# Kernel tuning notes

Measured on AMD Instinct MI355X. Metric: run time of the kernel, lower is better.

Reference implementation:

```python
import jax, jax.numpy as jnp
import numpy as np

N = 50000   # nodes
E = 800000  # edges (avg degree 16)
FIN = 128   # input node features
H = 4       # heads (conv1, conv2)
C = 64      # hidden_channels (per-head out dim)
SLOPE = 0.2
LN_EPS = 1e-5


def gatv2(x, src, dst, Wl, bl, Wr, br, att, bo, heads, outc, n):
    # GATv2Conv: e = att . LeakyReLU(x_l[src] + x_r[dst]); segment-softmax over dst; scatter-add alpha * x_l[src]
    xl = (x @ Wl + bl).reshape(n, heads, outc)
    xr = (x @ Wr + br).reshape(n, heads, outc)
    e = jax.nn.leaky_relu(xl[src] + xr[dst], SLOPE)          # [E, H, C]
    score = jnp.einsum('ehc,hc->eh', e, att)                 # [E, H]
    smax = jax.ops.segment_max(score, dst, num_segments=n)   # [N, H]
    ex = jnp.exp(score - smax[dst])
    denom = jax.ops.segment_sum(ex, dst, num_segments=n)
    alpha = ex / (denom[dst] + 1e-16)                        # [E, H]
    out = jax.ops.segment_sum(alpha[:, :, None] * xl[src], dst, num_segments=n)  # [N, H, C]
    return out.reshape(n, heads * outc) + bo                 # concat=True (default)


def layernorm(x, g, b):
    mu = x.mean(-1, keepdims=True)
    var = ((x - mu) ** 2).mean(-1, keepdims=True)
    return (x - mu) * jax.lax.rsqrt(var + LN_EPS) * g + b


def setup_inputs() -> dict:
    key = jax.random.key(0)
    ks = jax.random.split(key, 32)
    f32 = jnp.float32
    def nrm(k, shape, s):
        return jax.random.normal(k, shape, dtype=f32) * s
    inp = {}
    inp['x'] = jax.random.normal(ks[0], (N, FIN), dtype=f32)
    inp['edge_index'] = jax.random.randint(ks[1], (2, E), 0, N, dtype=jnp.int32)
    inp['batch'] = jnp.zeros((N,), dtype=jnp.int32)
    # conv1: 128 -> 4*64
    inp['W1l'] = nrm(ks[2], (FIN, H * C), 1.0 / np.sqrt(FIN))
    inp['b1l'] = jnp.zeros((H * C,), f32)
    inp['W1r'] = nrm(ks[3], (FIN, H * C), 1.0 / np.sqrt(FIN))
    inp['b1r'] = jnp.zeros((H * C,), f32)
    inp['a1'] = nrm(ks[4], (H, C), 1.0 / np.sqrt(C))
    inp['bo1'] = jnp.zeros((H * C,), f32)
    inp['ln1_g'] = jnp.ones((H * C,), f32)
    inp['ln1_b'] = jnp.zeros((H * C,), f32)
    # conv2: 256 -> 4*64
    inp['W2l'] = nrm(ks[5], (H * C, H * C), 1.0 / np.sqrt(H * C))
    inp['b2l'] = jnp.zeros((H * C,), f32)
    inp['W2r'] = nrm(ks[6], (H * C, H * C), 1.0 / np.sqrt(H * C))
    inp['b2r'] = jnp.zeros((H * C,), f32)
    inp['a2'] = nrm(ks[7], (H, C), 1.0 / np.sqrt(C))
    inp['bo2'] = jnp.zeros((H * C,), f32)
    inp['ln2_g'] = jnp.ones((H * C,), f32)
    inp['ln2_b'] = jnp.zeros((H * C,), f32)
    # conv3: 256 -> 1*64 (heads=1)
    inp['W3l'] = nrm(ks[8], (H * C, C), 1.0 / np.sqrt(H * C))
    inp['b3l'] = jnp.zeros((C,), f32)
    inp['W3r'] = nrm(ks[9], (H * C, C), 1.0 / np.sqrt(H * C))
    inp['b3r'] = jnp.zeros((C,), f32)
    inp['a3'] = nrm(ks[10], (1, C), 1.0 / np.sqrt(C))
    inp['bo3'] = jnp.zeros((C,), f32)
    inp['ln3_g'] = jnp.ones((C,), f32)
    inp['ln3_b'] = jnp.zeros((C,), f32)
    # final linear 64 -> 64
    inp['linW'] = nrm(ks[11], (C, C), 1.0 / np.sqrt(C))
    inp['linb'] = jnp.zeros((C,), f32)
    return inp


def reference(x, edge_index, batch,
              W1l, b1l, W1r, b1r, a1, bo1, ln1_g, ln1_b,
              W2l, b2l, W2r, b2r, a2, bo2, ln2_g, ln2_b,
              W3l, b3l, W3r, b3r, a3, bo3, ln3_g, ln3_b,
              linW, linb):
    src, dst = edge_index[0], edge_index[1]
    n = x.shape[0]
    h = gatv2(x, src, dst, W1l, b1l, W1r, b1r, a1, bo1, H, C, n)
    h = layernorm(h, ln1_g, ln1_b)
    h = gatv2(h, src, dst, W2l, b2l, W2r, b2r, a2, bo2, H, C, n)
    h = layernorm(h, ln2_g, ln2_b)
    h = gatv2(h, src, dst, W3l, b3l, W3r, b3r, a3, bo3, 1, C, n)
    h = layernorm(h, ln3_g, ln3_b)
    return h @ linW + linb
```

## Files before the change

kernel.cpp:

```cpp
#include <hip/hip_runtime.h>
#include <math.h>

#define LRELU_SLOPE 0.2f
#define L2E 1.4426950408889634f

typedef __attribute__((ext_vector_type(8))) short bf16x8;
typedef __attribute__((ext_vector_type(4))) float f32x4;
typedef __attribute__((ext_vector_type(2))) float f2;

__device__ __forceinline__ float fast_exp2(float x) {
  float r; asm("v_exp_f32 %0, %1" : "=v"(r) : "v"(x)); return r;
}

template<int CTRL>
__device__ __forceinline__ float dpp_add(float v) {
  int p = __builtin_amdgcn_update_dpp(0, __float_as_int(v), CTRL, 0xF, 0xF, true);
  return v + __int_as_float(p);
}
__device__ __forceinline__ float row16_sum(float v) {
  v = dpp_add<0xB1>(v);
  v = dpp_add<0x4E>(v);
  v = dpp_add<0x124>(v);
  v = dpp_add<0x128>(v);
  return v;
}

__device__ __forceinline__ unsigned short f2bf(float f) {
  unsigned u = __float_as_uint(f);
  return (unsigned short)((u + 0x7FFFu + ((u >> 16) & 1u)) >> 16);
}
__device__ __forceinline__ f2 bfpair(unsigned p) {
  f2 r;
  r.x = __uint_as_float(p << 16);
  r.y = __uint_as_float(p & 0xffff0000u);
  return r;
}

__global__ void wt_cvt_all(
    const float* __restrict__ W1l, const float* __restrict__ W1r,
    const float* __restrict__ W2l, const float* __restrict__ W2r,
    const float* __restrict__ W3l, const float* __restrict__ W3r,
    unsigned short* __restrict__ Wt1l, unsigned short* __restrict__ Wt1r,
    unsigned short* __restrict__ Wt2l, unsigned short* __restrict__ Wt2r,
    unsigned short* __restrict__ Wt3l, unsigned short* __restrict__ Wt3r) {
  const float* W; unsigned short* Wt; int K, N;
  switch (blockIdx.y) {
    case 0: W = W1l; Wt = Wt1l; K = 128; N = 256; break;
    case 1: W = W1r; Wt = Wt1r; K = 128; N = 256; break;
    case 2: W = W2l; Wt = Wt2l; K = 256; N = 256; break;
    case 3: W = W2r; Wt = Wt2r; K = 256; N = 256; break;
    case 4: W = W3l; Wt = Wt3l; K = 256; N = 64;  break;
    default: W = W3r; Wt = Wt3r; K = 256; N = 64; break;
  }
  int i = blockIdx.x * blockDim.x + threadIdx.x;
  int k8s = K / 8;
  int n = i / k8s, k8 = i - n * k8s;
  if (n >= N) return;
  unsigned short tmp[8];
#pragma unroll
  for (int j = 0; j < 8; ++j) tmp[j] = f2bf(W[(size_t)(k8 * 8 + j) * N + n]);
  *(bf16x8*)(Wt + (size_t)n * K + k8 * 8) = *(bf16x8*)tmp;
}

template<int K, bool CVT>
__global__ __launch_bounds__(256) void gemm_side(
    const void* __restrict__ Xsrc,
    const unsigned short* __restrict__ Wt0, const unsigned short* __restrict__ Wt1,
    const float* __restrict__ bias0, const float* __restrict__ bias1,
    unsigned short* __restrict__ Y0, unsigned short* __restrict__ Y1, int M) {
  constexpr int LDK = K + 8;
  constexpr int SMEM = (64 * LDK > 64 * 256) ? 64 * LDK : 64 * 256;
  __shared__ unsigned short smem[SMEM];
  unsigned short* As = smem;
  const int t = threadIdx.x, w = t >> 6, l = t & 63;
  const int lr = l & 15, lk = l >> 4;
  const int rowBase = blockIdx.x * 64;
  const int side = blockIdx.y;
  const unsigned short* Wt = side ? Wt1 : Wt0;
  const float* bias = side ? bias1 : bias0;
  unsigned short* Y = side ? Y1 : Y0;

  if constexpr (CVT) {
    const float* Xf = (const float*)Xsrc;
    constexpr int SPR = K / 4;
    constexpr int ITER = (64 * SPR) / 256;
#pragma unroll
    for (int i = 0; i < ITER; ++i) {
      int idx = i * 256 + t;
      int row = idx / SPR, seg = idx - row * SPR;
      int gr = rowBase + row; if (gr >= M) gr = M - 1;
      float4 v = *(const float4*)(Xf + (size_t)gr * K + seg * 4);
      ushort4 o;
      o.x = f2bf(v.x); o.y = f2bf(v.y); o.z = f2bf(v.z); o.w = f2bf(v.w);
      *(ushort4*)(As + row * LDK + seg * 4) = o;
    }
  } else {
    const unsigned short* Xb = (const unsigned short*)Xsrc;
    constexpr int SPR = K / 8;
    constexpr int ITER = (64 * SPR) / 256;
#pragma unroll
    for (int i = 0; i < ITER; ++i) {
      int idx = i * 256 + t;
      int row = idx / SPR, seg = idx - row * SPR;
      int gr = rowBase + row; if (gr >= M) gr = M - 1;
      *(uint4*)(As + row * LDK + seg * 8) = *(const uint4*)(Xb + (size_t)gr * K + seg * 8);
    }
  }
  __syncthreads();

  const int n0 = w * 64;

  f32x4 acc[4][4];
#pragma unroll
  for (int rt = 0; rt < 4; ++rt)
#pragma unroll
    for (int nt = 0; nt < 4; ++nt) acc[rt][nt] = (f32x4){0.f, 0.f, 0.f, 0.f};

  const unsigned short* bp = Wt + (size_t)(n0 + lr) * K + lk * 8;
  const unsigned short* ap = As + lr * LDK + lk * 8;

#pragma unroll
  for (int k0 = 0; k0 < K; k0 += 32) {
    bf16x8 a[4], b[4];
#pragma unroll
    for (int rt = 0; rt < 4; ++rt) a[rt] = *(const bf16x8*)(ap + rt * 16 * LDK + k0);
#pragma unroll
    for (int nt = 0; nt < 4; ++nt) b[nt] = *(const bf16x8*)(bp + nt * 16 * K + k0);
#pragma unroll
    for (int rt = 0; rt < 4; ++rt)
#pragma unroll
      for (int nt = 0; nt < 4; ++nt)
        acc[rt][nt] = __builtin_amdgcn_mfma_f32_16x16x32_bf16(a[rt], b[nt], acc[rt][nt], 0, 0, 0);
  }

  unsigned short* ybuf = smem;
  __syncthreads();
#pragma unroll
  for (int nt = 0; nt < 4; ++nt) {
    float bv = bias[n0 + nt * 16 + lr];
#pragma unroll
    for (int rt = 0; rt < 4; ++rt)
#pragma unroll
      for (int r = 0; r < 4; ++r)
        ybuf[(rt * 16 + lk * 4 + r) * 256 + n0 + nt * 16 + lr] =
            f2bf(acc[rt][nt][r] + bv);
  }
  __syncthreads();
#pragma unroll
  for (int i = 0; i < 8; ++i) {
    int boff = (i * 256 + t) * 16;
    int row = boff >> 9;
    int col = boff & 511;
    int rg = rowBase + row;
    if (rg < M)
      *(uint4*)((char*)Y + (((size_t)rg << 9) + col)) =
          *(const uint4*)((const char*)ybuf + boff);
  }
}

template<int K>
__global__ __launch_bounds__(256) void gemm_n64(
    const unsigned short* __restrict__ Xb,
    const unsigned short* __restrict__ Wt0, const unsigned short* __restrict__ Wt1,
    const float* __restrict__ bias0, const float* __restrict__ bias1,
    unsigned short* __restrict__ Y0, unsigned short* __restrict__ Y1, int M) {
  __shared__ unsigned short ybuf[64 * 64];
  const int side = blockIdx.y;
  const unsigned short* Wt = side ? Wt1 : Wt0;
  const float* bias = side ? bias1 : bias0;
  unsigned short* Y = side ? Y1 : Y0;
  const int t = threadIdx.x, w = t >> 6, l = t & 63;
  const int lr = l & 15, lk = l >> 4;
  const int rowBase = blockIdx.x * 64 + w * 16;

  f32x4 acc[4];
#pragma unroll
  for (int nt = 0; nt < 4; ++nt) acc[nt] = (f32x4){0.f, 0.f, 0.f, 0.f};

  int arow = rowBase + lr; if (arow >= M) arow = M - 1;
  const unsigned short* ap = Xb + (size_t)arow * K + lk * 8;
  const unsigned short* bp = Wt + (size_t)lr * K + lk * 8;

#pragma unroll
  for (int k0 = 0; k0 < K; k0 += 32) {
    bf16x8 a = *(const bf16x8*)(ap + k0);
    bf16x8 b[4];
#pragma unroll
    for (int nt = 0; nt < 4; ++nt) b[nt] = *(const bf16x8*)(bp + nt * 16 * K + k0);
#pragma unroll
    for (int nt = 0; nt < 4; ++nt)
      acc[nt] = __builtin_amdgcn_mfma_f32_16x16x32_bf16(a, b[nt], acc[nt], 0, 0, 0);
  }

#pragma unroll
  for (int nt = 0; nt < 4; ++nt) {
    float bv = bias[nt * 16 + lr];
#pragma unroll
    for (int r = 0; r < 4; ++r)
      ybuf[(w * 16 + lk * 4 + r) * 64 + nt * 16 + lr] = f2bf(acc[nt][r] + bv);
  }
  __syncthreads();

  const size_t base = (size_t)blockIdx.x * 64 * 64;
#pragma unroll
  for (int i = 0; i < 2; ++i) {
    int idx = i * 256 + t;
    int off = idx * 8;
    int row = off >> 6;
    if (blockIdx.x * 64 + row < M)
      *(uint4*)(Y + base + off) = *(const uint4*)(ybuf + off);
  }
}

__global__ void hist_deg(const int* __restrict__ dst, int* __restrict__ deg, int Ee) {
  int e = blockIdx.x * blockDim.x + threadIdx.x;
  if (e < Ee) atomicAdd(&deg[dst[e]], 1);
}

__global__ void scan_blk(const int* __restrict__ deg, int* __restrict__ rowptr,
                         int* __restrict__ bsum, int n) {
  __shared__ int sm[256];
  const int b = blockIdx.x, t = threadIdx.x;
  const int i = b * 256 + t;
  const int v = (i < n) ? deg[i] : 0;
  sm[t] = v;
  __syncthreads();
#pragma unroll
  for (int off = 1; off < 256; off <<= 1) {
    int x = (t >= off) ? sm[t - off] : 0;
    __syncthreads();
    sm[t] += x;
    __syncthreads();
  }
  if (i < n) rowptr[i] = sm[t] - v;
  if (t == 255) bsum[b] = sm[255];
}

__global__ void scan_top(const int* __restrict__ bsum, int* __restrict__ boff,
                         int* __restrict__ rowptr, int nb, int n) {
  __shared__ int sm[1024];
  const int t = threadIdx.x;
  const int v = (t < nb) ? bsum[t] : 0;
  sm[t] = v;
  __syncthreads();
#pragma unroll
  for (int off = 1; off < 1024; off <<= 1) {
    int x = (t >= off) ? sm[t - off] : 0;
    __syncthreads();
    sm[t] += x;
    __syncthreads();
  }
  if (t < nb) boff[t] = sm[t] - v;
  if (t == 1023) rowptr[n] = sm[1023];
}

__global__ void scan_add(int* __restrict__ rowptr, const int* __restrict__ boff, int n) {
  int i = blockIdx.x * 256 + threadIdx.x;
  if (i < n) rowptr[i] += boff[blockIdx.x];
}

__global__ void fill_csr(const int* __restrict__ src, const int* __restrict__ dst,
                         const int* __restrict__ rowptr, int* __restrict__ deg,
                         int* __restrict__ csr_src, int Ee) {
  int e = blockIdx.x * blockDim.x + threadIdx.x;
  if (e < Ee) {
    int d = dst[e];
    int p = atomicSub(&deg[d], 1) - 1;
    csr_src[rowptr[d] + p] = src[e];
  } else if (e < Ee + 16) {
    csr_src[e] = 0;
  }
}

__global__ __launch_bounds__(256) void gat_fused4(
    const unsigned short* __restrict__ xlb, const unsigned short* __restrict__ xrb,
    const float* __restrict__ att,
    const int* __restrict__ rowptr, const int* __restrict__ csr_src,
    const float* __restrict__ bo, const float* __restrict__ gam,
    const float* __restrict__ bet, unsigned short* __restrict__ outp, int n) {
  const int t = threadIdx.x;
  const int wv = t >> 6, lane = t & 63;
  const int node = blockIdx.x * 4 + wv;
  if (node >= n) return;
  const int cb = lane * 4;
  const unsigned loff = (unsigned)lane << 3;
  const char* xl8 = (const char*)xlb;

  uint2 xp = *(const uint2*)((const char*)xrb + (((unsigned)node << 9) + loff));
  const f2 xr0 = bfpair(xp.x), xr1 = bfpair(xp.y);
  const float4 a4 = *(const float4*)(att + cb);
  const f2 at0 = {a4.x * L2E, a4.y * L2E};
  const f2 at1 = {a4.z * L2E, a4.w * L2E};

  const int r0 = rowptr[node], r1 = rowptr[node + 1];
  float s = 0.f;
  f2 o0 = {0.f, 0.f}, o1 = {0.f, 0.f};

  if (r0 < r1) {
#define GOFF(idx) ((((unsigned)csr_src[idx]) << 9) + loff)
    uint2 p0 = *(const uint2*)(xl8 + GOFF(r0));
    uint2 p1 = *(const uint2*)(xl8 + GOFF(r0 + 1));
    uint2 p2 = *(const uint2*)(xl8 + GOFF(r0 + 2));
    uint2 p3 = *(const uint2*)(xl8 + GOFF(r0 + 3));
    for (int i = r0; i < r1; i += 4) {
      const uint2 c0 = p0, c1 = p1, c2 = p2, c3 = p3;
      if (i + 4 < r1) {
        p0 = *(const uint2*)(xl8 + GOFF(i + 4));
        p1 = *(const uint2*)(xl8 + GOFF(i + 5));
        p2 = *(const uint2*)(xl8 + GOFF(i + 6));
        p3 = *(const uint2*)(xl8 + GOFF(i + 7));
      }
      const f2 v00 = bfpair(c0.x), v01 = bfpair(c0.y);
      const f2 v10 = bfpair(c1.x), v11 = bfpair(c1.y);
      const f2 v20 = bfpair(c2.x), v21 = bfpair(c2.y);
      const f2 v30 = bfpair(c3.x), v31 = bfpair(c3.y);

      f2 e;
      f2 q0, q1, q2, q3;
      e = v00 + xr0; e = __builtin_elementwise_max(e, e * LRELU_SLOPE); q0 = e * at0;
      e = v01 + xr1; e = __builtin_elementwise_max(e, e * LRELU_SLOPE); q0 += e * at1;
      e = v10 + xr0; e = __builtin_elementwise_max(e, e * LRELU_SLOPE); q1 = e * at0;
      e = v11 + xr1; e = __builtin_elementwise_max(e, e * LRELU_SLOPE); q1 += e * at1;
      e = v20 + xr0; e = __builtin_elementwise_max(e, e * LRELU_SLOPE); q2 = e * at0;
      e = v21 + xr1; e = __builtin_elementwise_max(e, e * LRELU_SLOPE); q2 += e * at1;
      e = v30 + xr0; e = __builtin_elementwise_max(e, e * LRELU_SLOPE); q3 = e * at0;
      e = v31 + xr1; e = __builtin_elementwise_max(e, e * LRELU_SLOPE); q3 += e * at1;

      float s0 = row16_sum(q0.x + q0.y);
      float s1 = row16_sum(q1.x + q1.y);
      float s2 = row16_sum(q2.x + q2.y);
      float s3 = row16_sum(q3.x + q3.y);
      if (i + 1 >= r1) s1 = -INFINITY;
      if (i + 2 >= r1) s2 = -INFINITY;
      if (i + 3 >= r1) s3 = -INFINITY;
      const float w0 = fast_exp2(s0), w1 = fast_exp2(s1);
      const float w2 = fast_exp2(s2), w3 = fast_exp2(s3);
      s += (w0 + w1) + (w2 + w3);
      o0 += v00 * w0; o1 += v01 * w0;
      o0 += v10 * w1; o1 += v11 * w1;
      o0 += v20 * w2; o1 += v21 * w2;
      o0 += v30 * w3; o1 += v31 * w3;
    }
#undef GOFF
  }

  const float inv = 1.f / (s + 1e-16f);
  const float4 b4 = *(const float4*)(bo + cb);
  const float v0 = fmaf(o0.x, inv, b4.x);
  const float v1 = fmaf(o0.y, inv, b4.y);
  const float v2 = fmaf(o1.x, inv, b4.z);
  const float v3 = fmaf(o1.y, inv, b4.w);

  float ls = row16_sum(v0 + v1 + v2 + v3);
  ls += __shfl_xor(ls, 16);
  ls += __shfl_xor(ls, 32);
  const float mu = ls * (1.f / 256.f);
  const float d0 = v0 - mu, d1 = v1 - mu, d2 = v2 - mu, d3 = v3 - mu;
  float q = row16_sum(d0 * d0 + d1 * d1 + d2 * d2 + d3 * d3);
  q += __shfl_xor(q, 16);
  q += __shfl_xor(q, 32);
  const float rs = rsqrtf(q * (1.f / 256.f) + 1e-5f);

  const float4 g4 = *(const float4*)(gam + cb);
  const float4 e4 = *(const float4*)(bet + cb);
  ushort4 res;
  res.x = f2bf(fmaf(d0 * rs, g4.x, e4.x));
  res.y = f2bf(fmaf(d1 * rs, g4.y, e4.y));
  res.z = f2bf(fmaf(d2 * rs, g4.z, e4.z));
  res.w = f2bf(fmaf(d3 * rs, g4.w, e4.w));
  *(ushort4*)((char*)outp + (((unsigned)node << 9) + loff)) = res;
}

__global__ __launch_bounds__(512) void gat1_lin(
    const unsigned short* __restrict__ xlb, const unsigned short* __restrict__ xrb,
    const float* __restrict__ att,
    const int* __restrict__ rowptr, const int* __restrict__ csr_src,
    const float* __restrict__ bo, const float* __restrict__ gam,
    const float* __restrict__ bet,
    const float* __restrict__ linW, const float* __restrict__ linb,
    float* __restrict__ outp, int n) {
  const int t = threadIdx.x;
  const int wv = t >> 6, lane = t & 63;
  const int grp = lane >> 3, c8 = lane & 7;
  __shared__ float lw[64][64];
  __shared__ float hbuf[8][64];
  for (int i = t; i < 4096; i += 512) lw[i >> 6][i & 63] = linW[i];

  const int node = blockIdx.x * 8 + wv;
  const bool active = node < n;
  const int cb = c8 * 8;
  const unsigned loff = (unsigned)c8 << 4;
  const char* xl8 = (const char*)xlb;

  f2 xr2[4];
  int r0 = 0, r1 = 0;
  if (active) {
    uint4 p = *(const uint4*)((const char*)xrb + (((unsigned)node << 7) + loff));
    xr2[0] = bfpair(p.x); xr2[1] = bfpair(p.y); xr2[2] = bfpair(p.z); xr2[3] = bfpair(p.w);
    r0 = rowptr[node];
    r1 = rowptr[node + 1];
  } else {
#pragma unroll
    for (int j = 0; j < 4; ++j) xr2[j] = (f2){0.f, 0.f};
  }
  f2 at2[4];
  {
    float4 a0 = *(const float4*)(att + cb);
    float4 a1 = *(const float4*)(att + cb + 4);
    at2[0] = (f2){a0.x * L2E, a0.y * L2E}; at2[1] = (f2){a0.z * L2E, a0.w * L2E};
    at2[2] = (f2){a1.x * L2E, a1.y * L2E}; at2[3] = (f2){a1.z * L2E, a1.w * L2E};
  }

  float s = 0.f;
  f2 o2[4];
#pragma unroll
  for (int j = 0; j < 4; ++j) o2[j] = (f2){0.f, 0.f};

  uint4 vpk = {0u, 0u, 0u, 0u};
  {
    int i0 = r0 + grp;
    if (i0 < r1) vpk = *(const uint4*)(xl8 + ((((unsigned)csr_src[i0]) << 7) + loff));
  }
  bool valid = (r0 + grp) < r1;

  for (int base = r0; base < r1; base += 8) {
    const uint4 pc = vpk;
    const bool vld = valid;
    int inext = base + 8 + grp;
    valid = inext < r1;
    if (valid) vpk = *(const uint4*)(xl8 + ((((unsigned)csr_src[inext]) << 7) + loff));

    f2 v0 = bfpair(pc.x), v1 = bfpair(pc.y), v2 = bfpair(pc.z), v3 = bfpair(pc.w);
    f2 e0 = v0 + xr2[0]; e0 = __builtin_elementwise_max(e0, e0 * LRELU_SLOPE);
    f2 e1 = v1 + xr2[1]; e1 = __builtin_elementwise_max(e1, e1 * LRELU_SLOPE);
    f2 e2 = v2 + xr2[2]; e2 = __builtin_elementwise_max(e2, e2 * LRELU_SLOPE);
    f2 e3 = v3 + xr2[3]; e3 = __builtin_elementwise_max(e3, e3 * LRELU_SLOPE);
    f2 sc2 = e0 * at2[0];
    sc2 += e1 * at2[1];
    sc2 += e2 * at2[2];
    sc2 += e3 * at2[3];
    float sc = sc2.x + sc2.y;
    sc = dpp_add<0xB1>(sc);
    sc = dpp_add<0x4E>(sc);
    sc += __shfl_xor(sc, 4);
    if (!vld) sc = -INFINITY;
    const float w = fast_exp2(sc);
    s += w;
    o2[0] += v0 * w;
    o2[1] += v1 * w;
    o2[2] += v2 * w;
    o2[3] += v3 * w;
  }

  float o[8] = {o2[0].x, o2[0].y, o2[1].x, o2[1].y, o2[2].x, o2[2].y, o2[3].x, o2[3].y};
#pragma unroll
  for (int off = 8; off < 64; off <<= 1) {
#pragma unroll
    for (int i = 0; i < 8; ++i) o[i] += __shfl_xor(o[i], off);
    s += __shfl_xor(s, off);
  }

  const float inv = 1.f / (s + 1e-16f);
  float val[8];
  {
    float4 b0 = *(const float4*)(bo + cb);
    float4 b1 = *(const float4*)(bo + cb + 4);
    val[0] = fmaf(o[0], inv, b0.x); val[1] = fmaf(o[1], inv, b0.y);
    val[2] = fmaf(o[2], inv, b0.z); val[3] = fmaf(o[3], inv, b0.w);
    val[4] = fmaf(o[4], inv, b1.x); val[5] = fmaf(o[5], inv, b1.y);
    val[6] = fmaf(o[6], inv, b1.z); val[7] = fmaf(o[7], inv, b1.w);
  }

  float ls = 0.f;
#pragma unroll
  for (int i = 0; i < 8; ++i) ls += val[i];
  ls = dpp_add<0xB1>(ls);
  ls = dpp_add<0x4E>(ls);
  ls += __shfl_xor(ls, 4);
  float mu = ls * (1.f / 64.f);
  float d[8], q = 0.f;
#pragma unroll
  for (int i = 0; i < 8; ++i) { d[i] = val[i] - mu; q = fmaf(d[i], d[i], q); }
  q = dpp_add<0xB1>(q);
  q = dpp_add<0x4E>(q);
  q += __shfl_xor(q, 4);
  float var = q * (1.f / 64.f);
  const float rs = rsqrtf(var + 1e-5f);

  if (grp == 0) {
    float4 g0 = *(const float4*)(gam + cb);
    float4 g1 = *(const float4*)(gam + cb + 4);
    float4 e0 = *(const float4*)(bet + cb);
    float4 e1 = *(const float4*)(bet + cb + 4);
    float* hb = &hbuf[wv][cb];
    hb[0] = fmaf(d[0] * rs, g0.x, e0.x); hb[1] = fmaf(d[1] * rs, g0.y, e0.y);
    hb[2] = fmaf(d[2] * rs, g0.z, e0.z); hb[3] = fmaf(d[3] * rs, g0.w, e0.w);
    hb[4] = fmaf(d[4] * rs, g1.x, e1.x); hb[5] = fmaf(d[5] * rs, g1.y, e1.y);
    hb[6] = fmaf(d[6] * rs, g1.z, e1.z); hb[7] = fmaf(d[7] * rs, g1.w, e1.w);
  }
  __syncthreads();

  float acc = linb[lane];
#pragma unroll 8
  for (int k = 0; k < 64; ++k) acc = fmaf(hbuf[wv][k], lw[k][lane], acc);
  if (active) outp[(size_t)node * 64 + lane] = acc;
}

extern "C" void kernel_launch(void* const* d_in, const int* in_sizes, int n_in,
                              void* d_out, int out_size, void* d_ws, size_t ws_size,
                              hipStream_t stream) {
  const float* x    = (const float*)d_in[0];
  const int*   eidx = (const int*)d_in[1];
  const int Nn = in_sizes[0] / 128;
  const int Ee = in_sizes[1] / 2;
  const int* src = eidx;
  const int* dst = eidx + Ee;

  const float* W1l = (const float*)d_in[3];  const float* b1l = (const float*)d_in[4];
  const float* W1r = (const float*)d_in[5];  const float* b1r = (const float*)d_in[6];
  const float* a1  = (const float*)d_in[7];  const float* bo1 = (const float*)d_in[8];
  const float* g1  = (const float*)d_in[9];  const float* be1 = (const float*)d_in[10];
  const float* W2l = (const float*)d_in[11]; const float* b2l = (const float*)d_in[12];
  const float* W2r = (const float*)d_in[13]; const float* b2r = (const float*)d_in[14];
  const float* a2  = (const float*)d_in[15]; const float* bo2 = (const float*)d_in[16];
  const float* g2  = (const float*)d_in[17]; const float* be2 = (const float*)d_in[18];
  const float* W3l = (const float*)d_in[19]; const float* b3l = (const float*)d_in[20];
  const float* W3r = (const float*)d_in[21]; const float* b3r = (const float*)d_in[22];
  const float* a3  = (const float*)d_in[23]; const float* bo3 = (const float*)d_in[24];
  const float* g3  = (const float*)d_in[25]; const float* be3 = (const float*)d_in[26];
  const float* linW = (const float*)d_in[27]; const float* linb = (const float*)d_in[28];

  char* ws = (char*)d_ws;
  unsigned short* xl   = (unsigned short*)ws; ws += (size_t)Nn * 256 * 2;
  unsigned short* xr   = (unsigned short*)ws; ws += (size_t)Nn * 256 * 2;
  unsigned short* Xb   = (unsigned short*)ws; ws += (size_t)Nn * 256 * 2;
  unsigned short* Wt1l = (unsigned short*)ws; ws += 256 * 128 * 2;
  unsigned short* Wt1r = (unsigned short*)ws; ws += 256 * 128 * 2;
  unsigned short* Wt2l = (unsigned short*)ws; ws += 256 * 256 * 2;
  unsigned short* Wt2r = (unsigned short*)ws; ws += 256 * 256 * 2;
  unsigned short* Wt3l = (unsigned short*)ws; ws += 64 * 256 * 2;
  unsigned short* Wt3r = (unsigned short*)ws; ws += 64 * 256 * 2;
  int*   deg    = (int*)ws;    ws += (size_t)Nn * 4;
  int*   rowptr = (int*)ws;    ws += (size_t)(Nn + 1) * 4;
  int*   bsum   = (int*)ws;    ws += 1024 * 4;
  int*   boff   = (int*)ws;    ws += 1024 * 4;
  int*   csr_src= (int*)ws;    ws += (size_t)(Ee + 16) * 4;

  const int eblk = (Ee + 255) / 256;
  const int nblk = (Nn + 255) / 256;

  hipMemsetAsync(deg, 0, (size_t)Nn * 4, stream);
  hist_deg<<<eblk, 256, 0, stream>>>(dst, deg, Ee);
  wt_cvt_all<<<dim3(32, 6), 256, 0, stream>>>(W1l, W1r, W2l, W2r, W3l, W3r,
                                              Wt1l, Wt1r, Wt2l, Wt2r, Wt3l, Wt3r);
  scan_blk<<<nblk, 256, 0, stream>>>(deg, rowptr, bsum, Nn);
  scan_top<<<1, 1024, 0, stream>>>(bsum, boff, rowptr, nblk, Nn);
  scan_add<<<nblk, 256, 0, stream>>>(rowptr, boff, Nn);
  fill_csr<<<(Ee + 16 + 255) / 256, 256, 0, stream>>>(src, dst, rowptr, deg, csr_src, Ee);

  const int gdblk = (Nn + 63) / 64;

  gemm_side<128, true><<<dim3(gdblk, 2), 256, 0, stream>>>(x, Wt1l, Wt1r, b1l, b1r, xl, xr, Nn);
  gat_fused4<<<(Nn + 3) / 4, 256, 0, stream>>>(xl, xr, a1, rowptr, csr_src, bo1, g1, be1, Xb, Nn);

  gemm_side<256, false><<<dim3(gdblk, 2), 256, 0, stream>>>(Xb, Wt2l, Wt2r, b2l, b2r, xl, xr, Nn);
  gat_fused4<<<(Nn + 3) / 4, 256, 0, stream>>>(xl, xr, a2, rowptr, csr_src, bo2, g2, be2, Xb, Nn);

  gemm_n64<256><<<dim3(gdblk, 2), 256, 0, stream>>>(Xb, Wt3l, Wt3r, b3l, b3r, xl, xr, Nn);
  gat1_lin<<<(Nn + 7) / 8, 512, 0, stream>>>(xl, xr, a3, rowptr, csr_src, bo3, g3, be3,
                                             linW, linb, (float*)d_out, Nn);
}
```

Measured before the change: 375.2 us.

## Split wave into two half-waves processing alternate edges with 16-byte gathers

The 4-head GAT aggregation kernel now has each 32-lane half-wave handle alternate edges, with each lane loading 8 bf16 features (16 bytes) instead of 4. Per-head score reductions shrink to 8-lane groups, and the two halves' partial sums are combined by cross-half shuffles at the end. The intent is to use wider vector loads and more gathers in flight per wave, cutting loop iterations per node. The cost is extra shuffles, more registers, and wasted lanes on nodes with odd or small degree.

```diff
diff --git a/kernel.cpp b/kernel.cpp
--- a/kernel.cpp
+++ b/kernel.cpp
@@ -22,6 +22,12 @@
   v = dpp_add<0x4E>(v);
   v = dpp_add<0x124>(v);
   v = dpp_add<0x128>(v);
+  return v;
+}
+__device__ __forceinline__ float grp8_sum(float v) {
+  v = dpp_add<0xB1>(v);
+  v = dpp_add<0x4E>(v);
+  v += __shfl_xor(v, 4);
   return v;
 }
 
@@ -282,93 +288,108 @@
   const int wv = t >> 6, lane = t & 63;
   const int node = blockIdx.x * 4 + wv;
   if (node >= n) return;
-  const int cb = lane * 4;
-  const unsigned loff = (unsigned)lane << 3;
+  const int half = lane >> 5;
+  const int c32 = lane & 31;
+  const int cb = c32 * 8;
+  const unsigned loff = (unsigned)c32 << 4;
   const char* xl8 = (const char*)xlb;
 
-  uint2 xp = *(const uint2*)((const char*)xrb + (((unsigned)node << 9) + loff));
-  const f2 xr0 = bfpair(xp.x), xr1 = bfpair(xp.y);
-  const float4 a4 = *(const float4*)(att + cb);
-  const f2 at0 = {a4.x * L2E, a4.y * L2E};
-  const f2 at1 = {a4.z * L2E, a4.w * L2E};
+  uint4 xp = *(const uint4*)((const char*)xrb + (((unsigned)node << 9) + loff));
+  const f2 xr0 = bfpair(xp.x), xr1 = bfpair(xp.y), xr2 = bfpair(xp.z), xr3 = bfpair(xp.w);
+  const float4 a0 = *(const float4*)(att + cb);
+  const float4 a1 = *(const float4*)(att + cb + 4);
+  const f2 at0 = {a0.x * L2E, a0.y * L2E};
+  const f2 at1 = {a0.z * L2E, a0.w * L2E};
+  const f2 at2 = {a1.x * L2E, a1.y * L2E};
+  const f2 at3 = {a1.z * L2E, a1.w * L2E};
 
   const int r0 = rowptr[node], r1 = rowptr[node + 1];
   float s = 0.f;
-  f2 o0 = {0.f, 0.f}, o1 = {0.f, 0.f};
+  f2 o0 = {0.f, 0.f}, o1 = {0.f, 0.f}, o2 = {0.f, 0.f}, o3 = {0.f, 0.f};
 
   if (r0 < r1) {
 #define GOFF(idx) ((((unsigned)csr_src[idx]) << 9) + loff)
-    uint2 p0 = *(const uint2*)(xl8 + GOFF(r0));
-    uint2 p1 = *(const uint2*)(xl8 + GOFF(r0 + 1));
-    uint2 p2 = *(const uint2*)(xl8 + GOFF(r0 + 2));
-    uint2 p3 = *(const uint2*)(xl8 + GOFF(r0 + 3));
-    for (int i = r0; i < r1; i += 4) {
-      const uint2 c0 = p0, c1 = p1, c2 = p2, c3 = p3;
-      if (i + 4 < r1) {
-        p0 = *(const uint2*)(xl8 + GOFF(i + 4));
-        p1 = *(const uint2*)(xl8 + GOFF(i + 5));
-        p2 = *(const uint2*)(xl8 + GOFF(i + 6));
-        p3 = *(const uint2*)(xl8 + GOFF(i + 7));
+    uint4 p0 = *(const uint4*)(xl8 + GOFF(r0 + 0 + half));
+    uint4 p1 = *(const uint4*)(xl8 + GOFF(r0 + 2 + half));
+    uint4 p2 = *(const uint4*)(xl8 + GOFF(r0 + 4 + half));
+    uint4 p3 = *(const uint4*)(xl8 + GOFF(r0 + 6 + half));
+    for (int i = r0; i < r1; i += 8) {
+      const uint4 c0 = p0, c1 = p1, c2 = p2, c3 = p3;
+      if (i + 8 < r1) {
+        p0 = *(const uint4*)(xl8 + GOFF(i + 8 + half));
+        p1 = *(const uint4*)(xl8 + GOFF(i + 10 + half));
+        p2 = *(const uint4*)(xl8 + GOFF(i + 12 + half));
+        p3 = *(const uint4*)(xl8 + GOFF(i + 14 + half));
       }
-      const f2 v00 = bfpair(c0.x), v01 = bfpair(c0.y);
-      const f2 v10 = bfpair(c1.x), v11 = bfpair(c1.y);
-      const f2 v20 = bfpair(c2.x), v21 = bfpair(c2.y);
-      const f2 v30 = bfpair(c3.x), v31 = bfpair(c3.y);
-
-      f2 e;
-      f2 q0, q1, q2, q3;
-      e = v00 + xr0; e = __builtin_elementwise_max(e, e * LRELU_SLOPE); q0 = e * at0;
-      e = v01 + xr1; e = __builtin_elementwise_max(e, e * LRELU_SLOPE); q0 += e * at1;
-      e = v10 + xr0; e = __builtin_elementwise_max(e, e * LRELU_SLOPE); q1 = e * at0;
-      e = v11 + xr1; e = __builtin_elementwise_max(e, e * LRELU_SLOPE); q1 += e * at1;
-      e = v20 + xr0; e = __builtin_elementwise_max(e, e * LRELU_SLOPE); q2 = e * at0;
-      e = v21 + xr1; e = __builtin_elementwise_max(e, e * LRELU_SLOPE); q2 += e * at1;
-      e = v30 + xr0; e = __builtin_elementwise_max(e, e * LRELU_SLOPE); q3 = e * at0;
-      e = v31 + xr1; e = __builtin_elementwise_max(e, e * LRELU_SLOPE); q3 += e * at1;
-
-      float s0 = row16_sum(q0.x + q0.y);
-      float s1 = row16_sum(q1.x + q1.y);
-      float s2 = row16_sum(q2.x + q2.y);
-      float s3 = row16_sum(q3.x + q3.y);
-      if (i + 1 >= r1) s1 = -INFINITY;
-      if (i + 2 >= r1) s2 = -INFINITY;
-      if (i + 3 >= r1) s3 = -INFINITY;
-      const float w0 = fast_exp2(s0), w1 = fast_exp2(s1);
-      const float w2 = fast_exp2(s2), w3 = fast_exp2(s3);
-      s += (w0 + w1) + (w2 + w3);
-      o0 += v00 * w0; o1 += v01 * w0;
-      o0 += v10 * w1; o1 += v11 * w1;
-      o0 += v20 * w2; o1 += v21 * w2;
-      o0 += v30 * w3; o1 += v31 * w3;
+#pragma unroll
+      for (int k = 0; k < 4; ++k) {
+        const uint4 ck = (k == 0) ? c0 : (k == 1) ? c1 : (k == 2) ? c2 : c3;
+        const f2 v0 = bfpair(ck.x), v1 = bfpair(ck.y);
+        const f2 v2 = bfpair(ck.z), v3 = bfpair(ck.w);
+        f2 e, q;
+        e = v0 + xr0; e = __builtin_elementwise_max(e, e * LRELU_SLOPE); q = e * at0;
+        e = v1 + xr1; e = __builtin_elementwise_max(e, e * LRELU_SLOPE); q += e * at1;
+        e = v2 + xr2; e = __builtin_elementwise_max(e, e * LRELU_SLOPE); q += e * at2;
+        e = v3 + xr3; e = __builtin_elementwise_max(e, e * LRELU_SLOPE); q += e * at3;
+        float sc = grp8_sum(q.x + q.y);
+        const int ek = i + 2 * k + half;
+        if (ek >= r1) sc = -INFINITY;
+        const float w = fast_exp2(sc);
+        s += w;
+        o0 += v0 * w;
+        o1 += v1 * w;
+        o2 += v2 * w;
+        o3 += v3 * w;
+      }
     }
 #undef GOFF
+    o0.x += __shfl_xor(o0.x, 32); o0.y += __shfl_xor(o0.y, 32);
+    o1.x += __shfl_xor(o1.x, 32); o1.y += __shfl_xor(o1.y, 32);
+    o2.x += __shfl_xor(o2.x, 32); o2.y += __shfl_xor(o2.y, 32);
+    o3.x += __shfl_xor(o3.x, 32); o3.y += __shfl_xor(o3.y, 32);
+    s += __shfl_xor(s, 32);
   }
 
   const float inv = 1.f / (s + 1e-16f);
-  const float4 b4 = *(const float4*)(bo + cb);
-  const float v0 = fmaf(o0.x, inv, b4.x);
-  const float v1 = fmaf(o0.y, inv, b4.y);
-  const float v2 = fmaf(o1.x, inv, b4.z);
-  const float v3 = fmaf(o1.y, inv, b4.w);
-
-  float ls = row16_sum(v0 + v1 + v2 + v3);
+  float val[8];
+  {
+    float4 b0 = *(const float4*)(bo + cb);
+    float4 b1 = *(const float4*)(bo + cb + 4);
+    val[0] = fmaf(o0.x, inv, b0.x); val[1] = fmaf(o0.y, inv, b0.y);
+    val[2] = fmaf(o1.x, inv, b0.z); val[3] = fmaf(o1.y, inv, b0.w);
+    val[4] = fmaf(o2.x, inv, b1.x); val[5] = fmaf(o2.y, inv, b1.y);
+    val[6] = fmaf(o3.x, inv, b1.z); val[7] = fmaf(o3.y, inv, b1.w);
+  }
+
+  float ls = 0.f;
+#pragma unroll
+  for (int i = 0; i < 8; ++i) ls += val[i];
+  ls = row16_sum(ls);
   ls += __shfl_xor(ls, 16);
-  ls += __shfl_xor(ls, 32);
   const float mu = ls * (1.f / 256.f);
-  const float d0 = v0 - mu, d1 = v1 - mu, d2 = v2 - mu, d3 = v3 - mu;
-  float q = row16_sum(d0 * d0 + d1 * d1 + d2 * d2 + d3 * d3);
+  float d[8], q = 0.f;
+#pragma unroll
+  for (int i = 0; i < 8; ++i) { d[i] = val[i] - mu; q = fmaf(d[i], d[i], q); }
+  q = row16_sum(q);
   q += __shfl_xor(q, 16);
-  q += __shfl_xor(q, 32);
   const float rs = rsqrtf(q * (1.f / 256.f) + 1e-5f);
 
-  const float4 g4 = *(const float4*)(gam + cb);
-  const float4 e4 = *(const float4*)(bet + cb);
-  ushort4 res;
-  res.x = f2bf(fmaf(d0 * rs, g4.x, e4.x));
-  res.y = f2bf(fmaf(d1 * rs, g4.y, e4.y));
-  res.z = f2bf(fmaf(d2 * rs, g4.z, e4.z));
-  res.w = f2bf(fmaf(d3 * rs, g4.w, e4.w));
-  *(ushort4*)((char*)outp + (((unsigned)node << 9) + loff)) = res;
+  if (half == 0) {
+    float4 g0 = *(const float4*)(gam + cb);
+    float4 g1 = *(const float4*)(gam + cb + 4);
+    float4 e0 = *(const float4*)(bet + cb);
+    float4 e1 = *(const float4*)(bet + cb + 4);
+    unsigned short rb[8];
+    rb[0] = f2bf(fmaf(d[0] * rs, g0.x, e0.x));
+    rb[1] = f2bf(fmaf(d[1] * rs, g0.y, e0.y));
+    rb[2] = f2bf(fmaf(d[2] * rs, g0.z, e0.z));
+    rb[3] = f2bf(fmaf(d[3] * rs, g0.w, e0.w));
+    rb[4] = f2bf(fmaf(d[4] * rs, g1.x, e1.x));
+    rb[5] = f2bf(fmaf(d[5] * rs, g1.y, e1.y));
+    rb[6] = f2bf(fmaf(d[6] * rs, g1.z, e1.z));
+    rb[7] = f2bf(fmaf(d[7] * rs, g1.w, e1.w));
+    *(bf16x8*)((char*)outp + (((unsigned)node << 9) + loff)) = *(bf16x8*)rb;
+  }
 }
 
 __global__ __launch_bounds__(512) void gat1_lin(
```

After: 374.7 us. Within noise of the previous version (-0.1%).
